# Performance work log

Measured on AMD Instinct MI355X. Metric: run time of the kernel, lower is better.

The kernel has to match this reference:

```python
import jax, jax.numpy as jnp
import numpy as np
import math

SCALES = (1, 2, 4)
GROUPS = 8
EPS = 1e-5
TEMPERATURE = 1.0


def bilinear_resize(x, out_h, out_w):
    # torch F.interpolate mode='bilinear', align_corners=False
    B, C, h, w = x.shape
    def coords(out, in_):
        c = (jnp.arange(out, dtype=x.dtype) + 0.5) * (in_ / out) - 0.5
        c = jnp.clip(c, 0.0, in_ - 1.0)
        i0 = jnp.floor(c).astype(jnp.int32)
        i1 = jnp.minimum(i0 + 1, in_ - 1)
        t = c - i0.astype(x.dtype)
        return i0, i1, t
    y0, y1, ty = coords(out_h, h)
    x0, x1, tx = coords(out_w, w)
    r0 = x[:, :, y0, :]
    r1 = x[:, :, y1, :]
    v00 = r0[:, :, :, x0]; v01 = r0[:, :, :, x1]
    v10 = r1[:, :, :, x0]; v11 = r1[:, :, :, x1]
    top = v00 * (1.0 - tx) + v01 * tx
    bot = v10 * (1.0 - tx) + v11 * tx
    return top * (1.0 - ty)[:, None] + bot * ty[:, None]


def group_norm(x, gamma, beta):
    B, C, H, W = x.shape
    xg = x.reshape(B, GROUPS, C // GROUPS, H, W)
    mu = xg.mean(axis=(2, 3, 4), keepdims=True)
    var = xg.var(axis=(2, 3, 4), keepdims=True)
    xn = ((xg - mu) * jax.lax.rsqrt(var + EPS)).reshape(B, C, H, W)
    return xn * gamma[None, :, None, None] + beta[None, :, None, None]


def setup_inputs() -> dict:
    key = jax.random.key(0)
    B, C, H, W = 4, 128, 64, 64
    inter = max(C // 4, 8)  # 32
    S = len(SCALES)
    ks = jax.random.split(key, 8)
    def xavier(k, shape, fan_in, fan_out):
        a = math.sqrt(6.0 / (fan_in + fan_out))
        return jax.random.uniform(k, shape, jnp.float32, -a, a)
    inp = {
        'x': jax.random.normal(ks[0], (B, C, H, W), jnp.float32),
        'gn_w': jnp.ones((S, C), jnp.float32),
        'gn_b': jnp.zeros((S, C), jnp.float32),
        'qw': xavier(ks[1], (S, inter, C), C, inter),
        'qb': jnp.zeros((S, inter), jnp.float32),
        'kw': xavier(ks[2], (S, inter, C), C, inter),
        'kb': jnp.zeros((S, inter), jnp.float32),
        'vw': xavier(ks[3], (S, inter, C), C, inter),
        'vb': jnp.zeros((S, inter), jnp.float32),
        'ow': xavier(ks[4], (S, C, inter), inter, C),
        'ob': jnp.zeros((S, C), jnp.float32),
        'gamma': jnp.full((S,), 0.1 / S, jnp.float32),
        'scale_weights': jnp.full((S,), 1.0 / S, jnp.float32),
    }
    return inp


def _forward(x, gn_w, gn_b, qw, qb, kw, kb, vw, vb, ow, ob, gamma, scale_weights):
    B, C, H, W = x.shape
    inter = qw.shape[1]
    inv_scale = 1.0 / (TEMPERATURE * math.sqrt(inter))
    outs = []
    for i, s in enumerate(SCALES):
        if s == 1:
            xs = x
        else:
            xs = x.reshape(B, C, H // s, s, W // s, s).mean(axis=(3, 5))
        h, w = xs.shape[2], xs.shape[3]
        N = h * w
        xn = group_norm(xs, gn_w[i], gn_b[i])
        # 1x1 convs as channel contractions
        q = (jnp.einsum('oc,bchw->bohw', qw[i], xn) + qb[i][None, :, None, None]).reshape(B, inter, N)
        k = (jnp.einsum('oc,bchw->bohw', kw[i], xn) + kb[i][None, :, None, None]).reshape(B, inter, N)
        v = (jnp.einsum('oc,bchw->bohw', vw[i], xn) + vb[i][None, :, None, None]).reshape(B, inter, N)
        logits = jnp.einsum('bin,bim->bnm', q, k) * inv_scale  # [B, N, N]
        attn = jax.nn.softmax(logits, axis=-1)
        att = jnp.einsum('bnm,bim->bin', attn, v).reshape(B, inter, h, w)
        o = jnp.einsum('ci,bihw->bchw', ow[i], att) + ob[i][None, :, None, None]
        y = gamma[i] * o + xs
        if s > 1:
            y = bilinear_resize(y, H, W)
        outs.append(y)
    wts = jax.nn.softmax(scale_weights, axis=0)
    fused = wts[0] * outs[0]
    for i in range(1, len(outs)):
        fused = fused + wts[i] * outs[i]
    return fused


def reference(x, gn_w, gn_b, qw, qb, kw, kb, vw, vb, ow, ob, gamma, scale_weights):
    return _forward(x, gn_w, gn_b, qw, qb, kw, kb, vw, vb, ow, ob, gamma, scale_weights)
```

## Files before the change

kernel.cpp:

```cpp
#include <hip/hip_runtime.h>
#include <math.h>

#define B 4
#define C 128
#define CPG 16
#define INTER 32
#define SPLIT 16
#define KS 4

#define N1 4096
#define N2 1024
#define N4 256

#define QOFF2 (B * N1 * 32)
#define QOFF4 (QOFF2 + B * N2 * 32)
#define QTOT  (QOFF4 + B * N4 * 32)
#define PAOFF2 (B * KS * 32 * N1)
#define PAOFF4 (PAOFF2 + B * KS * 32 * N2)
#define PATOT  (PAOFF4 + B * KS * 32 * N4)
#define PMOFF2 (B * KS * 2 * N1)
#define PMOFF4 (PMOFF2 + B * KS * 2 * N2)
#define PMTOT  (PMOFF4 + B * KS * 2 * N4)

#define QSCALE 0.25503490f

typedef unsigned short ushort_t;
typedef __attribute__((ext_vector_type(8))) short short8;
typedef __attribute__((ext_vector_type(4))) float f32x4;

__device__ __forceinline__ ushort_t f2bf(float f) {
    union { float f; unsigned u; } x; x.f = f;
    unsigned r = x.u + 0x7fffu + ((x.u >> 16) & 1u);
    return (ushort_t)(r >> 16);
}

__device__ __forceinline__ void scale_wts(const float* __restrict__ sw,
                                          float& w0, float& w1, float& w2) {
    float a = sw[0], b = sw[1], c = sw[2];
    float m = fmaxf(a, fmaxf(b, c));
    float e0 = __expf(a - m), e1 = __expf(b - m), e2 = __expf(c - m);
    float inv = 1.0f / (e0 + e1 + e2);
    w0 = e0 * inv; w1 = e1 * inv; w2 = e2 * inv;
}

__device__ __forceinline__ void block_reduce_write(float s, float q,
                                                   float* __restrict__ dst2) {
    __shared__ float rs[256], rq[256];
    rs[threadIdx.x] = s; rq[threadIdx.x] = q;
    __syncthreads();
    for (int st = 128; st > 0; st >>= 1) {
        if (threadIdx.x < st) {
            rs[threadIdx.x] += rs[threadIdx.x + st];
            rq[threadIdx.x] += rq[threadIdx.x + st];
        }
        __syncthreads();
    }
    if (threadIdx.x == 0) { dst2[0] = rs[0]; dst2[1] = rq[0]; }
}

__global__ __launch_bounds__(256) void pool_stats_kernel(const float* __restrict__ x,
                                                         float* __restrict__ xs2,
                                                         float* __restrict__ xs4,
                                                         float* __restrict__ part) {
    int bid = blockIdx.x;
    if (bid < 512) {
        int sp = bid & 15, bg = bid >> 4;
        const float* base = x + ((bg * CPG) << 12) + sp * 4096;
        float s = 0.0f, q = 0.0f;
        for (int i = threadIdx.x; i < 4096; i += 256) {
            float v = base[i];
            s += v; q += v * v;
        }
        block_reduce_write(s, q, part + bid * 2);
    } else if (bid < 1024) {
        int blk = bid - 512;
        int sp = blk & 15, bg = blk >> 4;
        int bc = bg * CPG + sp;
        const float* src = x + (bc << 12);
        float* dst = xs2 + (bc << 10);
        float s = 0.0f, q = 0.0f;
        for (int p = threadIdx.x; p < 1024; p += 256) {
            int oy = p >> 5, ox = p & 31;
            const float* s2 = src + oy * 128 + ox * 2;
            float v = (s2[0] + s2[1] + s2[64] + s2[65]) * 0.25f;
            dst[p] = v; s += v; q += v * v;
        }
        block_reduce_write(s, q, part + 1024 + blk * 2);
    } else {
        int blk = bid - 1024;
        int sp = blk & 15, bg = blk >> 4;
        int bc = bg * CPG + sp;
        const float* src = x + (bc << 12);
        float* dst = xs4 + (bc << 8);
        int p = threadIdx.x & 255;
        int oy = p >> 4, ox = p & 15;
        const float* s4 = src + oy * 256 + ox * 4;
        float v = 0.0f;
        #pragma unroll
        for (int dy = 0; dy < 4; ++dy)
            #pragma unroll
            for (int dx = 0; dx < 4; ++dx) v += s4[dy * 64 + dx];
        v *= 0.0625f;
        dst[p] = v;
        block_reduce_write(v, v * v, part + 2048 + blk * 2);
    }
}

template <int N, int NSH>
__device__ __forceinline__ void qkv_body(int bi, const float* __restrict__ xs,
    const float* __restrict__ part,
    const float* __restrict__ gn_w, const float* __restrict__ gn_b,
    const float* __restrict__ qw, const float* __restrict__ qb,
    const float* __restrict__ kw, const float* __restrict__ kb,
    const float* __restrict__ vw, const float* __restrict__ vb,
    ushort_t* __restrict__ q_bf, ushort_t* __restrict__ k_bf, ushort_t* __restrict__ v_bf) {
    const int nc = N >> 8;
    int nchunk = bi % nc; bi /= nc;
    int og = bi & 3; bi >>= 2;
    int proj = bi % 3; int b = bi / 3;
    const float* wp = (proj == 0) ? qw : ((proj == 1) ? kw : vw);
    const float* bp = (proj == 0) ? qb : ((proj == 1) ? kb : vb);
    __shared__ float wl[8 * 128];
    __shared__ float2 ss[128];
    {
        int t = threadIdx.x;
        #pragma unroll
        for (int r = 0; r < 4; ++r) {
            int e = r * 256 + t;
            int o = e >> 7, c0 = e & 127;
            wl[c0 * 8 + o] = wp[(og * 8 + o) * C + c0];
        }
        if (t < 128) {
            int c = t;
            int bg = b * 8 + (c >> 4);
            float s = 0.0f, q = 0.0f;
            #pragma unroll
            for (int sp = 0; sp < SPLIT; ++sp) {
                s += part[(bg * SPLIT + sp) * 2];
                q += part[(bg * SPLIT + sp) * 2 + 1];
            }
            float inv = 1.0f / (float)(CPG << NSH);
            float mu = s * inv;
            float var = q * inv - mu * mu;
            float a = rsqrtf(var + 1e-5f) * gn_w[c];
            float2 r; r.x = a; r.y = gn_b[c] - mu * a;
            ss[c] = r;
        }
    }
    __syncthreads();
    int n = nchunk * 256 + threadIdx.x;
    const float* xb = xs + ((size_t)(b * C) << NSH) + n;
    float acc[8];
    #pragma unroll
    for (int o = 0; o < 8; ++o) acc[o] = bp[og * 8 + o];
    #pragma unroll 2
    for (int c0 = 0; c0 < C; ++c0) {
        float raw = xb[(size_t)c0 << NSH];
        float2 s2 = ss[c0];
        float xv = fmaf(s2.x, raw, s2.y);
        const float4* wr = (const float4*)&wl[c0 * 8];
        float4 w0 = wr[0], w1 = wr[1];
        acc[0] += w0.x * xv; acc[1] += w0.y * xv; acc[2] += w0.z * xv; acc[3] += w0.w * xv;
        acc[4] += w1.x * xv; acc[5] += w1.y * xv; acc[6] += w1.z * xv; acc[7] += w1.w * xv;
    }
    if (proj < 2) {
        float fs = (proj == 0) ? QSCALE : 1.0f;
        ushort_t tmp[8];
        #pragma unroll
        for (int o = 0; o < 8; ++o) tmp[o] = f2bf(acc[o] * fs);
        ushort_t* dst = ((proj == 0) ? q_bf : k_bf) + ((size_t)(b * N + n)) * 32 + og * 8;
        *(uint4*)dst = *(const uint4*)tmp;
    } else {
        #pragma unroll
        for (int o = 0; o < 8; ++o)
            v_bf[((size_t)(b * 32 + og * 8 + o) << NSH) + n] = f2bf(acc[o]);
    }
}

__global__ __launch_bounds__(256) void qkv_all_kernel(const float* __restrict__ x,
    const float* __restrict__ xs2, const float* __restrict__ xs4,
    const float* __restrict__ part,
    const float* __restrict__ gn_w, const float* __restrict__ gn_b,
    const float* __restrict__ qw, const float* __restrict__ qb,
    const float* __restrict__ kw, const float* __restrict__ kb,
    const float* __restrict__ vw, const float* __restrict__ vb,
    ushort_t* __restrict__ qbf, ushort_t* __restrict__ kbf, ushort_t* __restrict__ vbf) {
    int bid = blockIdx.x;
    if (bid < 768) {
        qkv_body<N1, 12>(bid, x, part, gn_w, gn_b, qw, qb, kw, kb, vw, vb, qbf, kbf, vbf);
    } else if (bid < 960) {
        qkv_body<N2, 10>(bid - 768, xs2, part + 1024, gn_w + C, gn_b + C,
                         qw + INTER * C, qb + INTER, kw + INTER * C, kb + INTER,
                         vw + INTER * C, vb + INTER,
                         qbf + QOFF2, kbf + QOFF2, vbf + QOFF2);
    } else {
        qkv_body<N4, 8>(bid - 960, xs4, part + 2048, gn_w + 2 * C, gn_b + 2 * C,
                        qw + 2 * INTER * C, qb + 2 * INTER, kw + 2 * INTER * C, kb + 2 * INTER,
                        vw + 2 * INTER * C, vb + 2 * INTER,
                        qbf + QOFF4, kbf + QOFF4, vbf + QOFF4);
    }
}

template <int N, int NSH>
__device__ __forceinline__ void attn_body(int bi,
    const ushort_t* __restrict__ q_bf, const ushort_t* __restrict__ k_bf,
    const ushort_t* __restrict__ v_bf,
    float* __restrict__ pacc, float* __restrict__ pml,
    ushort_t* K_lds, ushort_t* V_lds, ushort_t* P_lds) {
    int ks = bi % KS; bi /= KS;
    const int nqc = N >> 6;
    int qc = bi % nqc; int b = bi / nqc;
    int tid = threadIdx.x;
    int l = tid & 63, w = tid >> 6, lq = l & 15, g = l >> 4;
    int q0 = qc * 64 + w * 16;

    short8 qf = *(const short8*)(q_bf + ((size_t)(b * N + q0 + lq)) * 32 + g * 8);
    f32x4 acco0 = {0.f, 0.f, 0.f, 0.f}, acco1 = {0.f, 0.f, 0.f, 0.f};
    float mrun = -3.0e38f, lrun = 0.0f;

    const int kchunk = N / KS;
    int kbase = ks * kchunk;
    const int ntiles = kchunk >> 6;
    ushort_t* Pw = P_lds + w * 16 * 64;

    const int krow = tid >> 2;
    const int kidx = krow * 32 + ((((tid & 3) * 16) ^ ((krow & 3) << 4)) >> 1);
    const int vrow = tid >> 3;
    const int vidx = vrow * 64 + ((((tid & 7) * 16) ^ ((vrow & 7) << 4)) >> 1);

    const uint4* ksrc = (const uint4*)(k_bf + ((size_t)(b * N + kbase + krow)) * 32 + (tid & 3) * 8);
    const uint4* vsrc = (const uint4*)(v_bf + (((size_t)(b * 32 + vrow)) << NSH) + kbase + (tid & 7) * 8);
    uint4 kreg = *ksrc, vreg = *vsrc;

    const int ksw = (g ^ (lq & 3)) << 3;
    const int vsw0 = ((g * 16) ^ ((lq & 7) << 4)) >> 1;
    const int vsw1 = ((64 + g * 16) ^ ((lq & 7) << 4)) >> 1;

    for (int t = 0; t < ntiles; ++t) {
        __syncthreads();
        *(uint4*)&K_lds[kidx] = kreg;
        *(uint4*)&V_lds[vidx] = vreg;
        __syncthreads();
        if (t + 1 < ntiles) {
            ksrc += 256; vsrc += 8;
            kreg = *ksrc; vreg = *vsrc;
        }

        f32x4 sa[4];
        #pragma unroll
        for (int kt = 0; kt < 4; ++kt) {
            short8 kf = *(const short8*)&K_lds[(kt * 16 + lq) * 32 + ksw];
            f32x4 z = {0.f, 0.f, 0.f, 0.f};
            sa[kt] = __builtin_amdgcn_mfma_f32_16x16x32_bf16(kf, qf, z, 0, 0, 0);
        }
        float s[16];
        #pragma unroll
        for (int kt = 0; kt < 4; ++kt) {
            s[kt * 4 + 0] = sa[kt][0]; s[kt * 4 + 1] = sa[kt][1];
            s[kt * 4 + 2] = sa[kt][2]; s[kt * 4 + 3] = sa[kt][3];
        }
        float t0 = fmaxf(fmaxf(s[0], s[1]), s[2]);
        float t1 = fmaxf(fmaxf(s[3], s[4]), s[5]);
        float t2 = fmaxf(fmaxf(s[6], s[7]), s[8]);
        float t3 = fmaxf(fmaxf(s[9], s[10]), s[11]);
        float t4 = fmaxf(fmaxf(s[12], s[13]), s[14]);
        float tmax = fmaxf(fmaxf(fmaxf(t0, t1), fmaxf(t2, t3)), fmaxf(t4, s[15]));
        tmax = fmaxf(tmax, __shfl_xor(tmax, 16, 64));
        tmax = fmaxf(tmax, __shfl_xor(tmax, 32, 64));
        float nm = fmaxf(mrun, tmax);
        float corr = exp2f(mrun - nm);
        float p[16];
        float psum = 0.0f;
        #pragma unroll
        for (int j = 0; j < 16; ++j) {
            p[j] = exp2f(s[j] - nm);
            psum += p[j];
        }
        psum += __shfl_xor(psum, 16, 64);
        psum += __shfl_xor(psum, 32, 64);
        lrun = lrun * corr + psum;
        mrun = nm;
        #pragma unroll
        for (int e = 0; e < 4; ++e) { acco0[e] *= corr; acco1[e] *= corr; }
        #pragma unroll
        for (int kt = 0; kt < 4; ++kt) {
            unsigned u01, u23;
            asm("v_cvt_pk_bf16_f32 %0, %1, %2" : "=v"(u01) : "v"(p[kt * 4 + 0]), "v"(p[kt * 4 + 1]));
            asm("v_cvt_pk_bf16_f32 %0, %1, %2" : "=v"(u23) : "v"(p[kt * 4 + 2]), "v"(p[kt * 4 + 3]));
            int poff = kt * 32 + g * 8;
            uint2 pv; pv.x = u01; pv.y = u23;
            *(uint2*)&Pw[lq * 64 + ((poff ^ ((lq & 7) << 4)) >> 1)] = pv;
        }
        {
            short8 pf0 = *(const short8*)&Pw[lq * 64 + vsw0];
            short8 vf00 = *(const short8*)&V_lds[lq * 64 + vsw0];
            short8 vf10 = *(const short8*)&V_lds[(16 + lq) * 64 + vsw0];
            acco0 = __builtin_amdgcn_mfma_f32_16x16x32_bf16(vf00, pf0, acco0, 0, 0, 0);
            acco1 = __builtin_amdgcn_mfma_f32_16x16x32_bf16(vf10, pf0, acco1, 0, 0, 0);
            short8 pf1 = *(const short8*)&Pw[lq * 64 + vsw1];
            short8 vf01 = *(const short8*)&V_lds[lq * 64 + vsw1];
            short8 vf11 = *(const short8*)&V_lds[(16 + lq) * 64 + vsw1];
            acco0 = __builtin_amdgcn_mfma_f32_16x16x32_bf16(vf01, pf1, acco0, 0, 0, 0);
            acco1 = __builtin_amdgcn_mfma_f32_16x16x32_bf16(vf11, pf1, acco1, 0, 0, 0);
        }
    }
    int n = q0 + lq;
    size_t pb_ = ((size_t)(b * KS + ks)) * 32;
    #pragma unroll
    for (int r = 0; r < 4; ++r) {
        pacc[(pb_ + (g * 4 + r)) * N + n]      = acco0[r];
        pacc[(pb_ + 16 + (g * 4 + r)) * N + n] = acco1[r];
    }
    if (g == 0) {
        pml[((size_t)(b * KS + ks) * 2) * N + n]     = mrun;
        pml[((size_t)(b * KS + ks) * 2 + 1) * N + n] = lrun;
    }
}

__global__ __launch_bounds__(256) void attn_all_kernel(
    const ushort_t* __restrict__ qbf, const ushort_t* __restrict__ kbf,
    const ushort_t* __restrict__ vbf,
    float* __restrict__ pacc, float* __restrict__ pml) {
    __shared__ ushort_t K_lds[64 * 32];
    __shared__ ushort_t V_lds[32 * 64];
    __shared__ ushort_t P_lds[4 * 16 * 64];
    int bid = blockIdx.x;
    if (bid < 1024) {
        attn_body<N1, 12>(bid, qbf, kbf, vbf, pacc, pml, K_lds, V_lds, P_lds);
    } else if (bid < 1280) {
        attn_body<N2, 10>(bid - 1024, qbf + QOFF2, kbf + QOFF2, vbf + QOFF2,
                          pacc + PAOFF2, pml + PMOFF2, K_lds, V_lds, P_lds);
    } else {
        attn_body<N4, 8>(bid - 1280, qbf + QOFF4, kbf + QOFF4, vbf + QOFF4,
                         pacc + PAOFF4, pml + PMOFF4, K_lds, V_lds, P_lds);
    }
}

template <int N, int NSH>
__device__ __forceinline__ void comb_oy_body(int tile, const float* __restrict__ pacc,
    const float* __restrict__ pml, const float* __restrict__ ow, const float* __restrict__ ob,
    const float* __restrict__ gamma, const float* __restrict__ xs,
    float* __restrict__ ydst, const float* __restrict__ sw,
    float* att_lds, float* ow_lds) {
    const int ntiles = N >> 5;
    int b = tile / ntiles;
    int n0 = (tile % ntiles) << 5;
    int t = threadIdx.x;
    {
        const float4* src = (const float4*)ow;
        float4* dst = (float4*)ow_lds;
        dst[t] = src[t]; dst[256 + t] = src[256 + t];
        dst[512 + t] = src[512 + t]; dst[768 + t] = src[768 + t];
    }
    {
        int o = t >> 3, j = t & 7;
        int n = n0 + j * 4;
        float4 mv[KS], lv[KS], av4[KS];
        float4 M = {-3.0e38f, -3.0e38f, -3.0e38f, -3.0e38f};
        #pragma unroll
        for (int k2 = 0; k2 < KS; ++k2) {
            mv[k2]  = *(const float4*)&pml[((size_t)(b * KS + k2) * 2) * N + n];
            lv[k2]  = *(const float4*)&pml[((size_t)(b * KS + k2) * 2 + 1) * N + n];
            av4[k2] = *(const float4*)&pacc[((size_t)(b * KS + k2) * INTER + o) * N + n];
            M.x = fmaxf(M.x, mv[k2].x); M.y = fmaxf(M.y, mv[k2].y);
            M.z = fmaxf(M.z, mv[k2].z); M.w = fmaxf(M.w, mv[k2].w);
        }
        float4 L = {0.f, 0.f, 0.f, 0.f}, A = {0.f, 0.f, 0.f, 0.f};
        #pragma unroll
        for (int k2 = 0; k2 < KS; ++k2) {
            float4 wg;
            wg.x = exp2f(mv[k2].x - M.x); wg.y = exp2f(mv[k2].y - M.y);
            wg.z = exp2f(mv[k2].z - M.z); wg.w = exp2f(mv[k2].w - M.w);
            L.x += lv[k2].x * wg.x; L.y += lv[k2].y * wg.y;
            L.z += lv[k2].z * wg.z; L.w += lv[k2].w * wg.w;
            A.x += av4[k2].x * wg.x; A.y += av4[k2].y * wg.y;
            A.z += av4[k2].z * wg.z; A.w += av4[k2].w * wg.w;
        }
        float4 r;
        r.x = A.x / L.x; r.y = A.y / L.y; r.z = A.z / L.z; r.w = A.w / L.w;
        *(float4*)&att_lds[o * 36 + j * 4] = r;
    }
    __syncthreads();
    {
        int n = t & 31, cg2 = t >> 5;
        float av[32];
        #pragma unroll
        for (int i = 0; i < 32; ++i) av[i] = att_lds[i * 36 + n];
        float gm = gamma[0];
        float wsc = 1.0f;
        if (sw) { float w0, w1, w2; scale_wts(sw, w0, w1, w2); wsc = w0; }
        const float* xsb = xs + ((size_t)(b * C + cg2 * 16) << NSH) + n0 + n;
        float* yb = ydst + ((size_t)(b * C + cg2 * 16) << NSH) + n0 + n;
        #pragma unroll 4
        for (int cc = 0; cc < 16; ++cc) {
            int c = cg2 * 16 + cc;
            const float4* wr = (const float4*)&ow_lds[c * 32];
            float a0 = 0.f, a1 = 0.f, a2 = 0.f, a3 = 0.f;
            #pragma unroll
            for (int i4 = 0; i4 < 8; ++i4) {
                float4 wv = wr[i4];
                a0 += wv.x * av[i4 * 4 + 0]; a1 += wv.y * av[i4 * 4 + 1];
                a2 += wv.z * av[i4 * 4 + 2]; a3 += wv.w * av[i4 * 4 + 3];
            }
            float o_ = ob[c] + ((a0 + a1) + (a2 + a3));
            float y = gm * o_ + xsb[(size_t)cc << NSH];
            yb[(size_t)cc << NSH] = wsc * y;
        }
    }
    __syncthreads();
}

__global__ __launch_bounds__(256) void comb_oy_all_kernel(const float* __restrict__ pacc,
    const float* __restrict__ pml,
    const float* __restrict__ ow, const float* __restrict__ ob,
    const float* __restrict__ gamma,
    const float* __restrict__ x, const float* __restrict__ xs2, const float* __restrict__ xs4,
    float* __restrict__ out, float* __restrict__ y2, float* __restrict__ y4,
    const float* __restrict__ sw) {
    __shared__ float att_lds[32 * 36];
    __shared__ float ow_lds[128 * 32];
    int bid = blockIdx.x;
    if (bid < 512) {
        comb_oy_body<N1, 12>(bid, pacc, pml, ow, ob, gamma, x, out, sw, att_lds, ow_lds);
    } else if (bid < 640) {
        comb_oy_body<N2, 10>(bid - 512, pacc + PAOFF2, pml + PMOFF2,
                             ow + C * INTER, ob + C, gamma + 1, xs2, y2, nullptr,
                             att_lds, ow_lds);
    } else {
        comb_oy_body<N4, 8>(bid - 640, pacc + PAOFF4, pml + PMOFF4,
                            ow + 2 * C * INTER, ob + 2 * C, gamma + 2, xs4, y4, nullptr,
                            att_lds, ow_lds);
    }
}

__device__ __forceinline__ float bilerp(const float* __restrict__ img, int in,
                                        int oy, int ox, float r) {
    float cy = (oy + 0.5f) * r - 0.5f;
    cy = fminf(fmaxf(cy, 0.0f), (float)(in - 1));
    float cx = (ox + 0.5f) * r - 0.5f;
    cx = fminf(fmaxf(cx, 0.0f), (float)(in - 1));
    int y0 = (int)cy; int y1i = (y0 + 1 < in) ? y0 + 1 : in - 1; float ty = cy - (float)y0;
    int x0 = (int)cx; int x1i = (x0 + 1 < in) ? x0 + 1 : in - 1; float tx = cx - (float)x0;
    float v00 = img[y0 * in + x0];
    float v01 = img[y0 * in + x1i];
    float v10 = img[y1i * in + x0];
    float v11 = img[y1i * in + x1i];
    float top = v00 * (1.0f - tx) + v01 * tx;
    float bot = v10 * (1.0f - tx) + v11 * tx;
    return top * (1.0f - ty) + bot * ty;
}

__global__ __launch_bounds__(256) void fuse_kernel(float* __restrict__ out,
                                                   const float* __restrict__ y2,
                                                   const float* __restrict__ y4,
                                                   const float* __restrict__ sw) {
    int idx = blockIdx.x * 256 + threadIdx.x;
    int p = idx & 4095;
    int bc = idx >> 12;
    int oy = p >> 6, ox = p & 63;
    float w0, w1, w2; scale_wts(sw, w0, w1, w2);
    float v2 = bilerp(y2 + bc * 1024, 32, oy, ox, 0.5f);
    float v4 = bilerp(y4 + bc * 256, 16, oy, ox, 0.25f);
    out[idx] = out[idx] + w1 * v2 + w2 * v4;
}

extern "C" void kernel_launch(void* const* d_in, const int* in_sizes, int n_in,
                              void* d_out, int out_size, void* d_ws, size_t ws_size,
                              hipStream_t stream) {
    const float* x     = (const float*)d_in[0];
    const float* gn_w  = (const float*)d_in[1];
    const float* gn_b  = (const float*)d_in[2];
    const float* qw    = (const float*)d_in[3];
    const float* qb    = (const float*)d_in[4];
    const float* kw    = (const float*)d_in[5];
    const float* kb    = (const float*)d_in[6];
    const float* vw    = (const float*)d_in[7];
    const float* vb    = (const float*)d_in[8];
    const float* ow    = (const float*)d_in[9];
    const float* ob    = (const float*)d_in[10];
    const float* gamma = (const float*)d_in[11];
    const float* sw    = (const float*)d_in[12];
    float* out = (float*)d_out;

    float* ws    = (float*)d_ws;
    float* xs2   = ws;
    float* xs4   = xs2 + 524288;
    float* y2    = xs4 + 131072;
    float* y4    = y2 + 524288;
    float* part  = y4 + 131072;
    float* pacc  = part + 3072;
    float* pml   = pacc + PATOT;
    ushort_t* qbf = (ushort_t*)(pml + PMTOT);
    ushort_t* kbf = qbf + QTOT;
    ushort_t* vbf = kbf + QTOT;

    pool_stats_kernel<<<1536, 256, 0, stream>>>(x, xs2, xs4, part);
    qkv_all_kernel<<<1008, 256, 0, stream>>>(x, xs2, xs4, part, gn_w, gn_b,
                                             qw, qb, kw, kb, vw, vb, qbf, kbf, vbf);
    attn_all_kernel<<<1344, 256, 0, stream>>>(qbf, kbf, vbf, pacc, pml);
    comb_oy_all_kernel<<<672, 256, 0, stream>>>(pacc, pml, ow, ob, gamma,
                                                x, xs2, xs4, out, y2, y4, sw);
    fuse_kernel<<<8192, 256, 0, stream>>>(out, y2, y4, sw);
}
```

Baseline: 85.68 us.

## Process two query tiles per wave in attention and defer softmax rescaling

```diff
diff --git a/kernel.cpp b/kernel.cpp
--- a/kernel.cpp
+++ b/kernel.cpp
@@ -6,7 +6,8 @@
 #define CPG 16
 #define INTER 32
 #define SPLIT 16
-#define KS 4
+#define KS1 8
+#define KS24 4
 
 #define N1 4096
 #define N2 1024
@@ -15,12 +16,12 @@
 #define QOFF2 (B * N1 * 32)
 #define QOFF4 (QOFF2 + B * N2 * 32)
 #define QTOT  (QOFF4 + B * N4 * 32)
-#define PAOFF2 (B * KS * 32 * N1)
-#define PAOFF4 (PAOFF2 + B * KS * 32 * N2)
-#define PATOT  (PAOFF4 + B * KS * 32 * N4)
-#define PMOFF2 (B * KS * 2 * N1)
-#define PMOFF4 (PMOFF2 + B * KS * 2 * N2)
-#define PMTOT  (PMOFF4 + B * KS * 2 * N4)
+#define PAOFF2 (B * KS1 * 32 * N1)
+#define PAOFF4 (PAOFF2 + B * KS24 * 32 * N2)
+#define PATOT  (PAOFF4 + B * KS24 * 32 * N4)
+#define PMOFF2 (B * KS1 * 2 * N1)
+#define PMOFF4 (PMOFF2 + B * KS24 * 2 * N2)
+#define PMTOT  (PMOFF4 + B * KS24 * 2 * N4)
 
 #define QSCALE 0.25503490f
 
@@ -201,27 +202,70 @@
     }
 }
 
-template <int N, int NSH>
+#define SOFTMAX_PACK(sa, mrun, lrun, aA, aB, PwF)                                              \
+    {                                                                                          \
+        float s_[16];                                                                          \
+        _Pragma("unroll")                                                                      \
+        for (int kt = 0; kt < 4; ++kt) {                                                       \
+            s_[kt * 4 + 0] = sa[kt][0]; s_[kt * 4 + 1] = sa[kt][1];                            \
+            s_[kt * 4 + 2] = sa[kt][2]; s_[kt * 4 + 3] = sa[kt][3];                            \
+        }                                                                                      \
+        float t0 = fmaxf(fmaxf(s_[0], s_[1]), s_[2]);                                          \
+        float t1 = fmaxf(fmaxf(s_[3], s_[4]), s_[5]);                                          \
+        float t2 = fmaxf(fmaxf(s_[6], s_[7]), s_[8]);                                          \
+        float t3 = fmaxf(fmaxf(s_[9], s_[10]), s_[11]);                                        \
+        float t4 = fmaxf(fmaxf(s_[12], s_[13]), s_[14]);                                       \
+        float tmax = fmaxf(fmaxf(fmaxf(t0, t1), fmaxf(t2, t3)), fmaxf(t4, s_[15]));            \
+        tmax = fmaxf(tmax, __shfl_xor(tmax, 16, 64));                                          \
+        tmax = fmaxf(tmax, __shfl_xor(tmax, 32, 64));                                          \
+        if (!__all(tmax - mrun <= 8.0f)) {                                                     \
+            float nmx = fmaxf(mrun, tmax);                                                     \
+            float corr = exp2f(mrun - nmx);                                                    \
+            lrun *= corr;                                                                      \
+            _Pragma("unroll")                                                                  \
+            for (int e = 0; e < 4; ++e) { aA[e] *= corr; aB[e] *= corr; }                       \
+            mrun = nmx;                                                                        \
+        }                                                                                      \
+        float p_[16];                                                                          \
+        float psum = 0.0f;                                                                     \
+        _Pragma("unroll")                                                                      \
+        for (int j = 0; j < 16; ++j) { p_[j] = exp2f(s_[j] - mrun); psum += p_[j]; }           \
+        psum += __shfl_xor(psum, 16, 64);                                                      \
+        psum += __shfl_xor(psum, 32, 64);                                                      \
+        lrun += psum;                                                                          \
+        _Pragma("unroll")                                                                      \
+        for (int kt = 0; kt < 4; ++kt) {                                                       \
+            unsigned u01, u23;                                                                 \
+            asm("v_cvt_pk_bf16_f32 %0, %1, %2" : "=v"(u01) : "v"(p_[kt * 4 + 0]), "v"(p_[kt * 4 + 1])); \
+            asm("v_cvt_pk_bf16_f32 %0, %1, %2" : "=v"(u23) : "v"(p_[kt * 4 + 2]), "v"(p_[kt * 4 + 3])); \
+            uint2 pv; pv.x = u01; pv.y = u23;                                                  \
+            *(uint2*)&(PwF)[lq * 64 + (((kt * 32 + g * 8) ^ ((lq & 7) << 4)) >> 1)] = pv;      \
+        }                                                                                      \
+    }
+
+template <int N, int NSH, int KSL>
 __device__ __forceinline__ void attn_body(int bi,
     const ushort_t* __restrict__ q_bf, const ushort_t* __restrict__ k_bf,
     const ushort_t* __restrict__ v_bf,
     float* __restrict__ pacc, float* __restrict__ pml,
     ushort_t* K_lds, ushort_t* V_lds, ushort_t* P_lds) {
-    int ks = bi % KS; bi /= KS;
-    const int nqc = N >> 6;
+    int ks = bi % KSL; bi /= KSL;
+    const int nqc = N >> 7;
     int qc = bi % nqc; int b = bi / nqc;
     int tid = threadIdx.x;
     int l = tid & 63, w = tid >> 6, lq = l & 15, g = l >> 4;
-    int q0 = qc * 64 + w * 16;
-
-    short8 qf = *(const short8*)(q_bf + ((size_t)(b * N + q0 + lq)) * 32 + g * 8);
-    f32x4 acco0 = {0.f, 0.f, 0.f, 0.f}, acco1 = {0.f, 0.f, 0.f, 0.f};
-    float mrun = -3.0e38f, lrun = 0.0f;
-
-    const int kchunk = N / KS;
+    int q0 = qc * 128 + w * 32;
+
+    short8 qf0 = *(const short8*)(q_bf + ((size_t)(b * N + q0 + lq)) * 32 + g * 8);
+    short8 qf1 = *(const short8*)(q_bf + ((size_t)(b * N + q0 + 16 + lq)) * 32 + g * 8);
+    f32x4 a00 = {0.f, 0.f, 0.f, 0.f}, a01 = {0.f, 0.f, 0.f, 0.f};
+    f32x4 a10 = {0.f, 0.f, 0.f, 0.f}, a11 = {0.f, 0.f, 0.f, 0.f};
+    float m0 = -3.0e38f, l0 = 0.0f, m1 = -3.0e38f, l1 = 0.0f;
+
+    const int kchunk = N / KSL;
     int kbase = ks * kchunk;
     const int ntiles = kchunk >> 6;
-    ushort_t* Pw = P_lds + w * 16 * 64;
+    ushort_t* Pw = P_lds + w * (32 * 64);
 
     const int krow = tid >> 2;
     const int kidx = krow * 32 + ((((tid & 3) * 16) ^ ((krow & 3) << 4)) >> 1);
@@ -246,74 +290,48 @@
             kreg = *ksrc; vreg = *vsrc;
         }
 
-        f32x4 sa[4];
+        f32x4 sa0[4], sa1[4];
         #pragma unroll
         for (int kt = 0; kt < 4; ++kt) {
             short8 kf = *(const short8*)&K_lds[(kt * 16 + lq) * 32 + ksw];
             f32x4 z = {0.f, 0.f, 0.f, 0.f};
-            sa[kt] = __builtin_amdgcn_mfma_f32_16x16x32_bf16(kf, qf, z, 0, 0, 0);
-        }
-        float s[16];
-        #pragma unroll
-        for (int kt = 0; kt < 4; ++kt) {
-            s[kt * 4 + 0] = sa[kt][0]; s[kt * 4 + 1] = sa[kt][1];
-            s[kt * 4 + 2] = sa[kt][2]; s[kt * 4 + 3] = sa[kt][3];
-        }
-        float t0 = fmaxf(fmaxf(s[0], s[1]), s[2]);
-        float t1 = fmaxf(fmaxf(s[3], s[4]), s[5]);
-        float t2 = fmaxf(fmaxf(s[6], s[7]), s[8]);
-        float t3 = fmaxf(fmaxf(s[9], s[10]), s[11]);
-        float t4 = fmaxf(fmaxf(s[12], s[13]), s[14]);
-        float tmax = fmaxf(fmaxf(fmaxf(t0, t1), fmaxf(t2, t3)), fmaxf(t4, s[15]));
-        tmax = fmaxf(tmax, __shfl_xor(tmax, 16, 64));
-        tmax = fmaxf(tmax, __shfl_xor(tmax, 32, 64));
-        float nm = fmaxf(mrun, tmax);
-        float corr = exp2f(mrun - nm);
-        float p[16];
-        float psum = 0.0f;
-        #pragma unroll
-        for (int j = 0; j < 16; ++j) {
-            p[j] = exp2f(s[j] - nm);
-            psum += p[j];
-        }
-        psum += __shfl_xor(psum, 16, 64);
-        psum += __shfl_xor(psum, 32, 64);
-        lrun = lrun * corr + psum;
-        mrun = nm;
-        #pragma unroll
-        for (int e = 0; e < 4; ++e) { acco0[e] *= corr; acco1[e] *= corr; }
-        #pragma unroll
-        for (int kt = 0; kt < 4; ++kt) {
-            unsigned u01, u23;
-            asm("v_cvt_pk_bf16_f32 %0, %1, %2" : "=v"(u01) : "v"(p[kt * 4 + 0]), "v"(p[kt * 4 + 1]));
-            asm("v_cvt_pk_bf16_f32 %0, %1, %2" : "=v"(u23) : "v"(p[kt * 4 + 2]), "v"(p[kt * 4 + 3]));
-            int poff = kt * 32 + g * 8;
-            uint2 pv; pv.x = u01; pv.y = u23;
-            *(uint2*)&Pw[lq * 64 + ((poff ^ ((lq & 7) << 4)) >> 1)] = pv;
-        }
-        {
-            short8 pf0 = *(const short8*)&Pw[lq * 64 + vsw0];
-            short8 vf00 = *(const short8*)&V_lds[lq * 64 + vsw0];
-            short8 vf10 = *(const short8*)&V_lds[(16 + lq) * 64 + vsw0];
-            acco0 = __builtin_amdgcn_mfma_f32_16x16x32_bf16(vf00, pf0, acco0, 0, 0, 0);
-            acco1 = __builtin_amdgcn_mfma_f32_16x16x32_bf16(vf10, pf0, acco1, 0, 0, 0);
-            short8 pf1 = *(const short8*)&Pw[lq * 64 + vsw1];
-            short8 vf01 = *(const short8*)&V_lds[lq * 64 + vsw1];
-            short8 vf11 = *(const short8*)&V_lds[(16 + lq) * 64 + vsw1];
-            acco0 = __builtin_amdgcn_mfma_f32_16x16x32_bf16(vf01, pf1, acco0, 0, 0, 0);
-            acco1 = __builtin_amdgcn_mfma_f32_16x16x32_bf16(vf11, pf1, acco1, 0, 0, 0);
-        }
-    }
-    int n = q0 + lq;
-    size_t pb_ = ((size_t)(b * KS + ks)) * 32;
+            sa0[kt] = __builtin_amdgcn_mfma_f32_16x16x32_bf16(kf, qf0, z, 0, 0, 0);
+            sa1[kt] = __builtin_amdgcn_mfma_f32_16x16x32_bf16(kf, qf1, z, 0, 0, 0);
+        }
+        SOFTMAX_PACK(sa0, m0, l0, a00, a01, Pw)
+        SOFTMAX_PACK(sa1, m1, l1, a10, a11, (Pw + 16 * 64))
+
+        short8 vf00 = *(const short8*)&V_lds[lq * 64 + vsw0];
+        short8 vf10 = *(const short8*)&V_lds[(16 + lq) * 64 + vsw0];
+        short8 vf01 = *(const short8*)&V_lds[lq * 64 + vsw1];
+        short8 vf11 = *(const short8*)&V_lds[(16 + lq) * 64 + vsw1];
+        short8 p00 = *(const short8*)&Pw[lq * 64 + vsw0];
+        short8 p01 = *(const short8*)&Pw[lq * 64 + vsw1];
+        short8 p10 = *(const short8*)&Pw[(16 + lq) * 64 + vsw0];
+        short8 p11 = *(const short8*)&Pw[(16 + lq) * 64 + vsw1];
+        a00 = __builtin_amdgcn_mfma_f32_16x16x32_bf16(vf00, p00, a00, 0, 0, 0);
+        a01 = __builtin_amdgcn_mfma_f32_16x16x32_bf16(vf10, p00, a01, 0, 0, 0);
+        a00 = __builtin_amdgcn_mfma_f32_16x16x32_bf16(vf01, p01, a00, 0, 0, 0);
+        a01 = __builtin_amdgcn_mfma_f32_16x16x32_bf16(vf11, p01, a01, 0, 0, 0);
+        a10 = __builtin_amdgcn_mfma_f32_16x16x32_bf16(vf00, p10, a10, 0, 0, 0);
+        a11 = __builtin_amdgcn_mfma_f32_16x16x32_bf16(vf10, p10, a11, 0, 0, 0);
+        a10 = __builtin_amdgcn_mfma_f32_16x16x32_bf16(vf01, p11, a10, 0, 0, 0);
+        a11 = __builtin_amdgcn_mfma_f32_16x16x32_bf16(vf11, p11, a11, 0, 0, 0);
+    }
+    int n0 = q0 + lq, n1 = q0 + 16 + lq;
+    size_t pb_ = ((size_t)(b * KSL + ks)) * 32;
     #pragma unroll
     for (int r = 0; r < 4; ++r) {
-        pacc[(pb_ + (g * 4 + r)) * N + n]      = acco0[r];
-        pacc[(pb_ + 16 + (g * 4 + r)) * N + n] = acco1[r];
+        pacc[(pb_ + (g * 4 + r)) * N + n0]      = a00[r];
+        pacc[(pb_ + 16 + (g * 4 + r)) * N + n0] = a01[r];
+        pacc[(pb_ + (g * 4 + r)) * N + n1]      = a10[r];
+        pacc[(pb_ + 16 + (g * 4 + r)) * N + n1] = a11[r];
     }
     if (g == 0) {
-        pml[((size_t)(b * KS + ks) * 2) * N + n]     = mrun;
-        pml[((size_t)(b * KS + ks) * 2 + 1) * N + n] = lrun;
+        pml[((size_t)(b * KSL + ks) * 2) * N + n0]     = m0;
+        pml[((size_t)(b * KSL + ks) * 2 + 1) * N + n0] = l0;
+        pml[((size_t)(b * KSL + ks) * 2) * N + n1]     = m1;
+        pml[((size_t)(b * KSL + ks) * 2 + 1) * N + n1] = l1;
     }
 }
 
@@ -323,20 +341,20 @@
     float* __restrict__ pacc, float* __restrict__ pml) {
     __shared__ ushort_t K_lds[64 * 32];
     __shared__ ushort_t V_lds[32 * 64];
-    __shared__ ushort_t P_lds[4 * 16 * 64];
+    __shared__ ushort_t P_lds[4 * 32 * 64];
     int bid = blockIdx.x;
     if (bid < 1024) {
-        attn_body<N1, 12>(bid, qbf, kbf, vbf, pacc, pml, K_lds, V_lds, P_lds);
-    } else if (bid < 1280) {
-        attn_body<N2, 10>(bid - 1024, qbf + QOFF2, kbf + QOFF2, vbf + QOFF2,
-                          pacc + PAOFF2, pml + PMOFF2, K_lds, V_lds, P_lds);
+        attn_body<N1, 12, KS1>(bid, qbf, kbf, vbf, pacc, pml, K_lds, V_lds, P_lds);
+    } else if (bid < 1152) {
+        attn_body<N2, 10, KS24>(bid - 1024, qbf + QOFF2, kbf + QOFF2, vbf + QOFF2,
+                                pacc + PAOFF2, pml + PMOFF2, K_lds, V_lds, P_lds);
     } else {
-        attn_body<N4, 8>(bid - 1280, qbf + QOFF4, kbf + QOFF4, vbf + QOFF4,
-                         pacc + PAOFF4, pml + PMOFF4, K_lds, V_lds, P_lds);
-    }
-}
-
-template <int N, int NSH>
+        attn_body<N4, 8, KS24>(bid - 1152, qbf + QOFF4, kbf + QOFF4, vbf + QOFF4,
+                               pacc + PAOFF4, pml + PMOFF4, K_lds, V_lds, P_lds);
+    }
+}
+
+template <int N, int NSH, int KSL>
 __device__ __forceinline__ void comb_oy_body(int tile, const float* __restrict__ pacc,
     const float* __restrict__ pml, const float* __restrict__ ow, const float* __restrict__ ob,
     const float* __restrict__ gamma, const float* __restrict__ xs,
@@ -355,26 +373,26 @@
     {
         int o = t >> 3, j = t & 7;
         int n = n0 + j * 4;
-        float4 mv[KS], lv[KS], av4[KS];
+        float4 mv[KSL];
         float4 M = {-3.0e38f, -3.0e38f, -3.0e38f, -3.0e38f};
         #pragma unroll
-        for (int k2 = 0; k2 < KS; ++k2) {
-            mv[k2]  = *(const float4*)&pml[((size_t)(b * KS + k2) * 2) * N + n];
-            lv[k2]  = *(const float4*)&pml[((size_t)(b * KS + k2) * 2 + 1) * N + n];
-            av4[k2] = *(const float4*)&pacc[((size_t)(b * KS + k2) * INTER + o) * N + n];
+        for (int k2 = 0; k2 < KSL; ++k2) {
+            mv[k2] = *(const float4*)&pml[((size_t)(b * KSL + k2) * 2) * N + n];
             M.x = fmaxf(M.x, mv[k2].x); M.y = fmaxf(M.y, mv[k2].y);
             M.z = fmaxf(M.z, mv[k2].z); M.w = fmaxf(M.w, mv[k2].w);
         }
         float4 L = {0.f, 0.f, 0.f, 0.f}, A = {0.f, 0.f, 0.f, 0.f};
         #pragma unroll
-        for (int k2 = 0; k2 < KS; ++k2) {
+        for (int k2 = 0; k2 < KSL; ++k2) {
+            float4 lv = *(const float4*)&pml[((size_t)(b * KSL + k2) * 2 + 1) * N + n];
+            float4 av = *(const float4*)&pacc[((size_t)(b * KSL + k2) * INTER + o) * N + n];
             float4 wg;
             wg.x = exp2f(mv[k2].x - M.x); wg.y = exp2f(mv[k2].y - M.y);
             wg.z = exp2f(mv[k2].z - M.z); wg.w = exp2f(mv[k2].w - M.w);
-            L.x += lv[k2].x * wg.x; L.y += lv[k2].y * wg.y;
-            L.z += lv[k2].z * wg.z; L.w += lv[k2].w * wg.w;
-            A.x += av4[k2].x * wg.x; A.y += av4[k2].y * wg.y;
-            A.z += av4[k2].z * wg.z; A.w += av4[k2].w * wg.w;
+            L.x += lv.x * wg.x; L.y += lv.y * wg.y;
+            L.z += lv.z * wg.z; L.w += lv.w * wg.w;
+            A.x += av.x * wg.x; A.y += av.y * wg.y;
+            A.z += av.z * wg.z; A.w += av.w * wg.w;
         }
         float4 r;
         r.x = A.x / L.x; r.y = A.y / L.y; r.z = A.z / L.z; r.w = A.w / L.w;
@@ -421,15 +439,15 @@
     __shared__ float ow_lds[128 * 32];
     int bid = blockIdx.x;
     if (bid < 512) {
-        comb_oy_body<N1, 12>(bid, pacc, pml, ow, ob, gamma, x, out, sw, att_lds, ow_lds);
+        comb_oy_body<N1, 12, KS1>(bid, pacc, pml, ow, ob, gamma, x, out, sw, att_lds, ow_lds);
     } else if (bid < 640) {
-        comb_oy_body<N2, 10>(bid - 512, pacc + PAOFF2, pml + PMOFF2,
-                             ow + C * INTER, ob + C, gamma + 1, xs2, y2, nullptr,
-                             att_lds, ow_lds);
+        comb_oy_body<N2, 10, KS24>(bid - 512, pacc + PAOFF2, pml + PMOFF2,
+                                   ow + C * INTER, ob + C, gamma + 1, xs2, y2, nullptr,
+                                   att_lds, ow_lds);
     } else {
-        comb_oy_body<N4, 8>(bid - 640, pacc + PAOFF4, pml + PMOFF4,
-                            ow + 2 * C * INTER, ob + 2 * C, gamma + 2, xs4, y4, nullptr,
-                            att_lds, ow_lds);
+        comb_oy_body<N4, 8, KS24>(bid - 640, pacc + PAOFF4, pml + PMOFF4,
+                                  ow + 2 * C * INTER, ob + 2 * C, gamma + 2, xs4, y4, nullptr,
+                                  att_lds, ow_lds);
     }
 }
 
@@ -497,7 +515,7 @@
     pool_stats_kernel<<<1536, 256, 0, stream>>>(x, xs2, xs4, part);
     qkv_all_kernel<<<1008, 256, 0, stream>>>(x, xs2, xs4, part, gn_w, gn_b,
                                              qw, qb, kw, kb, vw, vb, qbf, kbf, vbf);
-    attn_all_kernel<<<1344, 256, 0, stream>>>(qbf, kbf, vbf, pacc, pml);
+    attn_all_kernel<<<1184, 256, 0, stream>>>(qbf, kbf, vbf, pacc, pml);
     comb_oy_all_kernel<<<672, 256, 0, stream>>>(pacc, pml, ow, ob, gamma,
                                                 x, xs2, xs4, out, y2, y4, sw);
     fuse_kernel<<<8192, 256, 0, stream>>>(out, y2, y4, sw);
```

New measurement: 85.25 us. No clear change (-0.5%).
